# Performance work log

Measured on AMD Instinct MI355X. Metric: run time of the kernel, lower is better.

Reference implementation:

```python
import jax, jax.numpy as jnp
import numpy as np

B, C, T, V = 64, 64, 128, 25   # batch, in_channels, frames, joints
R = 8                          # rel_channels = in_channels // rel_reduction
TS = 9                         # time_step (temporal taps of dynamic adjacency)
OUT = 64                       # out_channels (conv3)


def setup_inputs() -> dict:
    key = jax.random.key(0)
    ks = jax.random.split(key, 10)
    p = lambda k, shape: jax.random.normal(k, shape, jnp.float32) * 0.05
    return {
        'x':  jax.random.normal(ks[0], (B, C, T, V), jnp.float32),
        'A':  jax.random.normal(ks[1], (V, V), jnp.float32) * 0.1,
        'W1': p(ks[2], (R, C)),       'b1': p(ks[3], (R,)),
        'W2': p(ks[4], (R, C)),       'b2': p(ks[5], (R,)),
        'W4': p(ks[6], (C * TS, R)),  'b4': p(ks[7], (C * TS,)),
        'W3': p(ks[8], (OUT, C)),     'b3': p(ks[9], (OUT,)),
    }


def reference(x, A, W1, b1, W2, b2, W4, b4, W3, b3):
    alpha = 1.0
    # conv1/conv2: 1x1 Conv2d then mean over time (dim -2). 1x1 conv is linear,
    # so mean(conv(x)) == einsum/T + bias.  -> (B, R, V)
    x1 = jnp.einsum('rc,bctv->brv', W1, x) / T + b1[None, :, None]
    x2 = jnp.einsum('rc,bctv->brv', W2, x) / T + b2[None, :, None]
    # tanh relation: (B, R, V, 1) - (B, R, 1, V) -> (B, R, V, V)
    rel = jnp.tanh(x1[:, :, :, None] - x2[:, :, None, :])
    # conv4 (1x1): rel_channels -> C*TS dynamic adjacency, + static A
    Adyn = jnp.einsum('or,brij->boij', W4, rel) + b4[None, :, None, None]
    Adyn = Adyn * alpha + A[None, None]                      # (B, C*TS, V, V)
    # reshape(B, C, TS, V, V).permute(0,1,3,4,2): per-(b,c) temporal graph kernel
    Wk = Adyn.reshape(B, C, TS, V, V).transpose(0, 1, 3, 4, 2)  # (B, C, V, V, TS)
    # x -> (B, C, V, T), causal left-pad by TS-1 (matches F.pad(x, (TS-1, 0)))
    xp = jnp.pad(x.transpose(0, 1, 3, 2), ((0, 0), (0, 0), (0, 0), (TS - 1, 0)))
    # Grouped conv1d loop over V vertices, fused into TS tap-wise einsums:
    # z[b,c,t,i] = sum_{v,k} xp[b,c,v,t+k] * Wk[b,c,v,i,k]   (stride=1)
    z = jnp.zeros((B, C, T, V), x.dtype)
    for k in range(TS):  # small fixed tap loop
        z = z + jnp.einsum('bcvt,bcvi->bcti', xp[..., k:k + T], Wk[..., k])
    # conv3: 1x1 Conv2d C -> OUT
    out = jnp.einsum('oc,bctv->botv', W3, z) + b3[None, :, None, None]
    return out
```

## Files before the change

### kernel.cpp

```cpp
#include <hip/hip_runtime.h>
#include <hip/hip_bf16.h>

#define BB 64
#define CC 64
#define TT_ 128
#define VV 25
#define RR 8
#define TS_ 9
#define OO 64

typedef __hip_bfloat16 bf16;
typedef __attribute__((ext_vector_type(8))) short short8;
typedef __attribute__((ext_vector_type(4))) float f32x4;

__device__ __forceinline__ unsigned short f2b(float f) {
    bf16 h = __float2bfloat16(f);
    return __builtin_bit_cast(unsigned short, h);
}

__global__ __launch_bounds__(256) void k_mean(const float* __restrict__ x,
                                              float* __restrict__ xm) {
    __shared__ float sm[256];
    int bc = blockIdx.x;
    int tid = threadIdx.x;
    const float* p = x + (size_t)bc * TT_ * VV;
    float s = 0.f;
    if (tid < 250) {
        for (int off = tid; off < TT_ * VV; off += 250) s += p[off];
    }
    sm[tid] = s;
    __syncthreads();
    if (tid < VV) {
        float tot = 0.f;
        #pragma unroll
        for (int g = 0; g < 10; g++) tot += sm[g * VV + tid];
        xm[bc * VV + tid] = tot * (1.0f / TT_);
    }
}

__global__ __launch_bounds__(256) void k_rel(const float* __restrict__ xm,
                                             const float* __restrict__ W1,
                                             const float* __restrict__ b1,
                                             const float* __restrict__ W2,
                                             const float* __restrict__ b2,
                                             float* __restrict__ rel,
                                             const float* __restrict__ W3,
                                             const float* __restrict__ b3,
                                             float* __restrict__ w3t,
                                             float* __restrict__ b3f) {
    int tid = threadIdx.x;
    if (blockIdx.x >= BB) {
        int idx = (blockIdx.x - BB) * 256 + tid;
        if (idx < OO * CC) {
            int o = idx / CC, c = idx % CC;
            w3t[c * OO + o] = W3[idx];
        }
        if (idx < OO) b3f[idx] = b3[idx];
        return;
    }
    __shared__ float x1s[RR][VV];
    __shared__ float x2s[RR][VV];
    int b = blockIdx.x;
    for (int idx = tid; idx < RR * VV; idx += 256) {
        int r = idx / VV, v = idx % VV;
        float s1 = b1[r], s2 = b2[r];
        for (int c = 0; c < CC; c++) {
            float xv = xm[(b * CC + c) * VV + v];
            s1 += W1[r * CC + c] * xv;
            s2 += W2[r * CC + c] * xv;
        }
        x1s[r][v] = s1;
        x2s[r][v] = s2;
    }
    __syncthreads();
    float* relb = rel + (size_t)b * VV * VV * RR;
    for (int idx = tid; idx < VV * VV * RR; idx += 256) {
        int r = idx % RR;
        int i = (idx / RR) % VV;
        int v = idx / (RR * VV);
        relb[idx] = tanhf(x1s[r][v] - x2s[r][i]);
    }
}

__global__ __launch_bounds__(256) void k_z(const float* __restrict__ x,
                                           const float* __restrict__ Ag,
                                           const float* __restrict__ W4,
                                           const float* __restrict__ b4,
                                           const float* __restrict__ rel,
                                           bf16* __restrict__ zws) {
    __shared__ __align__(16) unsigned short xpadB[136 * 40];
    __shared__ __align__(16) unsigned short AdbS[TS_ * 32 * 40];
    __shared__ float w4l[TS_][RR];
    __shared__ float b4l[TS_];

    int tid = threadIdx.x;
    int bc = blockIdx.x;
    int b = bc / CC, c = bc % CC;

    if (tid < TS_ * RR)
        w4l[tid / RR][tid % RR] = W4[(c * TS_ + tid / RR) * RR + tid % RR];
    if (tid < TS_) b4l[tid] = b4[c * TS_ + tid];

    if (tid < 128) ((unsigned int*)xpadB)[(tid >> 4) * 20 + (tid & 15)] = 0u;
    for (int id = tid; id < 128 * 7; id += 256) {
        int r = 8 + id / 7, v = 25 + id % 7;
        xpadB[r * 40 + v] = 0;
    }
    for (int id = tid; id < TS_ * 25 * 7; id += 256) {
        int s = id / 175, rem = id % 175;
        int i = rem / 7, v = 25 + rem % 7;
        AdbS[(s * 32 + i) * 40 + v] = 0;
    }
    for (int id = tid; id < TS_ * 7 * 16; id += 256) {
        int s = id / 112, rem = id % 112;
        int i = 25 + rem / 16, u = rem % 16;
        ((unsigned int*)AdbS)[(s * 32 + i) * 20 + u] = 0u;
    }
    const float4* xg4 = (const float4*)(x + (size_t)bc * TT_ * VV);
    for (int i4 = tid; i4 < TT_ * VV / 4; i4 += 256) {
        float4 f = xg4[i4];
        int idx = i4 * 4;
        float fe[4] = {f.x, f.y, f.z, f.w};
        #pragma unroll
        for (int e = 0; e < 4; e++) {
            int t = (idx + e) / VV, v = (idx + e) % VV;
            xpadB[(t + 8) * 40 + v] = f2b(fe[e]);
        }
    }
    __syncthreads();

    const float* relb = rel + (size_t)b * VV * VV * RR;
    for (int task = tid; task < VV * VV; task += 256) {
        int v = task / VV, i = task % VV;
        const float4* r4 = (const float4*)(relb + (size_t)task * RR);
        float4 ra = r4[0], rb_ = r4[1];
        float av = Ag[task];
        #pragma unroll
        for (int s = 0; s < TS_; s++) {
            float a2 = b4l[s] + av;
            a2 += w4l[s][0] * ra.x + w4l[s][1] * ra.y + w4l[s][2] * ra.z + w4l[s][3] * ra.w;
            a2 += w4l[s][4] * rb_.x + w4l[s][5] * rb_.y + w4l[s][6] * rb_.z + w4l[s][7] * rb_.w;
            AdbS[(s * 32 + i) * 40 + v] = f2b(a2);
        }
    }
    __syncthreads();

    int lane = tid & 63, wv = tid >> 6;
    int ml = lane & 15, qd = lane >> 4;
    f32x4 acc00 = {0.f, 0.f, 0.f, 0.f};
    f32x4 acc01 = acc00, acc10 = acc00, acc11 = acc00;
    int rowA0 = (wv * 2) * 16 + ml;
    #pragma unroll
    for (int s = 0; s < TS_; s++) {
        short8 a0 = *(const short8*)&xpadB[(rowA0 + s) * 40 + qd * 8];
        short8 a1 = *(const short8*)&xpadB[(rowA0 + 16 + s) * 40 + qd * 8];
        short8 b0 = *(const short8*)&AdbS[(s * 32 + ml) * 40 + qd * 8];
        short8 b1 = *(const short8*)&AdbS[(s * 32 + 16 + ml) * 40 + qd * 8];
        acc00 = __builtin_amdgcn_mfma_f32_16x16x32_bf16(a0, b0, acc00, 0, 0, 0);
        acc01 = __builtin_amdgcn_mfma_f32_16x16x32_bf16(a0, b1, acc01, 0, 0, 0);
        acc10 = __builtin_amdgcn_mfma_f32_16x16x32_bf16(a1, b0, acc10, 0, 0, 0);
        acc11 = __builtin_amdgcn_mfma_f32_16x16x32_bf16(a1, b1, acc11, 0, 0, 0);
    }

    bf16* zb = zws + (size_t)bc * TT_ * VV;
    int t0 = (wv * 2) * 16 + qd * 4;
    int i0 = ml, i1 = 16 + ml;
    #pragma unroll
    for (int r = 0; r < 4; r++) {
        zb[(t0 + r) * VV + i0]      = __float2bfloat16(acc00[r]);
        zb[(t0 + 16 + r) * VV + i0] = __float2bfloat16(acc10[r]);
    }
    if (i1 < VV) {
        #pragma unroll
        for (int r = 0; r < 4; r++) {
            zb[(t0 + r) * VV + i1]      = __float2bfloat16(acc01[r]);
            zb[(t0 + 16 + r) * VV + i1] = __float2bfloat16(acc11[r]);
        }
    }
}

__global__ __launch_bounds__(256) void k_conv3(const bf16* __restrict__ zws,
                                               const float* __restrict__ w3t,
                                               const float* __restrict__ b3f,
                                               float* __restrict__ out) {
    __shared__ float zl[CC][128];
    __shared__ float w3l[CC * OO];
    int tid = threadIdx.x;
    int b = blockIdx.x / 25, tile = blockIdx.x % 25;
    int tj0 = tile * 128;

    for (int idx = tid; idx < CC * OO; idx += 256) w3l[idx] = w3t[idx];
    for (int idx = tid; idx < CC * 128; idx += 256) {
        int c = idx >> 7, j = idx & 127;
        zl[c][j] = __bfloat162float(zws[(size_t)(b * CC + c) * (TT_ * VV) + tj0 + j]);
    }
    __syncthreads();

    int og = tid >> 5, tg = tid & 31;
    int o0 = og * 8, j0 = tg * 4;
    float accv[8][4];
    #pragma unroll
    for (int a = 0; a < 8; a++)
        #pragma unroll
        for (int q = 0; q < 4; q++) accv[a][q] = 0.f;

    for (int c = 0; c < CC; c++) {
        float4 zv = *(const float4*)&zl[c][j0];
        float4 wa = *(const float4*)&w3l[c * OO + o0];
        float4 wb = *(const float4*)&w3l[c * OO + o0 + 4];
        float zq[4] = {zv.x, zv.y, zv.z, zv.w};
        float wo[8] = {wa.x, wa.y, wa.z, wa.w, wb.x, wb.y, wb.z, wb.w};
        #pragma unroll
        for (int a = 0; a < 8; a++)
            #pragma unroll
            for (int q = 0; q < 4; q++) accv[a][q] += wo[a] * zq[q];
    }

    #pragma unroll
    for (int a = 0; a < 8; a++) {
        int o = o0 + a;
        float bo = b3f[o];
        float4 res;
        res.x = accv[a][0] + bo;
        res.y = accv[a][1] + bo;
        res.z = accv[a][2] + bo;
        res.w = accv[a][3] + bo;
        *(float4*)(out + ((size_t)(b * OO + o)) * (TT_ * VV) + tj0 + j0) = res;
    }
}

extern "C" void kernel_launch(void* const* d_in, const int* in_sizes, int n_in,
                              void* d_out, int out_size, void* d_ws, size_t ws_size,
                              hipStream_t stream) {
    const float* x  = (const float*)d_in[0];
    const float* A  = (const float*)d_in[1];
    const float* W1 = (const float*)d_in[2];
    const float* b1 = (const float*)d_in[3];
    const float* W2 = (const float*)d_in[4];
    const float* b2 = (const float*)d_in[5];
    const float* W4 = (const float*)d_in[6];
    const float* b4 = (const float*)d_in[7];
    const float* W3 = (const float*)d_in[8];
    const float* b3 = (const float*)d_in[9];
    float* out = (float*)d_out;

    char* ws = (char*)d_ws;
    float* xm   = (float*)(ws);
    float* rel  = (float*)(ws + 409600);
    float* w3t  = (float*)(ws + 1689600);
    float* b3f  = (float*)(ws + 1705984);
    bf16*  zws  = (bf16*)(ws + 1706240);

    k_mean <<<BB * CC, 256, 0, stream>>>(x, xm);
    k_rel  <<<BB + 16, 256, 0, stream>>>(xm, W1, b1, W2, b2, rel, W3, b3, w3t, b3f);
    k_z    <<<BB * CC, 256, 0, stream>>>(x, A, W4, b4, rel, zws);
    k_conv3<<<BB * 25, 256, 0, stream>>>(zws, w3t, b3f, out);
}
```

Baseline: 194.8 us.

## Use bf16 MFMA for conv3 and drop weight-prep work from rel and z kernels

The 1x1 output conv (k_conv3) moves from a scalar fp32 FMA loop to bf16 16x16x32 MFMA tiles. It converts W3 to bf16 in shared memory inside the kernel and stages z as raw bf16 pairs. This removes the separate W3 transpose and bias copy that k_rel used to do in extra blocks. k_z now reads W4 and b4 straight from global instead of staging them in shared memory. It also drops one barrier and the zero-fill of the unused padding rows of the adjacency tile, whose results are never stored. The cost is lower precision from rounding W3 to bf16, plus narrower output stores: 16 contiguous floats per lane group instead of float4 per thread.

```diff
diff --git a/kernel.cpp b/kernel.cpp
--- a/kernel.cpp
+++ b/kernel.cpp
@@ -43,24 +43,10 @@
                                              const float* __restrict__ b1,
                                              const float* __restrict__ W2,
                                              const float* __restrict__ b2,
-                                             float* __restrict__ rel,
-                                             const float* __restrict__ W3,
-                                             const float* __restrict__ b3,
-                                             float* __restrict__ w3t,
-                                             float* __restrict__ b3f) {
-    int tid = threadIdx.x;
-    if (blockIdx.x >= BB) {
-        int idx = (blockIdx.x - BB) * 256 + tid;
-        if (idx < OO * CC) {
-            int o = idx / CC, c = idx % CC;
-            w3t[c * OO + o] = W3[idx];
-        }
-        if (idx < OO) b3f[idx] = b3[idx];
-        return;
-    }
+                                             float* __restrict__ rel) {
     __shared__ float x1s[RR][VV];
     __shared__ float x2s[RR][VV];
-    int b = blockIdx.x;
+    int b = blockIdx.x, tid = threadIdx.x;
     for (int idx = tid; idx < RR * VV; idx += 256) {
         int r = idx / VV, v = idx % VV;
         float s1 = b1[r], s2 = b2[r];
@@ -90,16 +76,10 @@
                                            bf16* __restrict__ zws) {
     __shared__ __align__(16) unsigned short xpadB[136 * 40];
     __shared__ __align__(16) unsigned short AdbS[TS_ * 32 * 40];
-    __shared__ float w4l[TS_][RR];
-    __shared__ float b4l[TS_];
 
     int tid = threadIdx.x;
     int bc = blockIdx.x;
     int b = bc / CC, c = bc % CC;
-
-    if (tid < TS_ * RR)
-        w4l[tid / RR][tid % RR] = W4[(c * TS_ + tid / RR) * RR + tid % RR];
-    if (tid < TS_) b4l[tid] = b4[c * TS_ + tid];
 
     if (tid < 128) ((unsigned int*)xpadB)[(tid >> 4) * 20 + (tid & 15)] = 0u;
     for (int id = tid; id < 128 * 7; id += 256) {
@@ -110,11 +90,6 @@
         int s = id / 175, rem = id % 175;
         int i = rem / 7, v = 25 + rem % 7;
         AdbS[(s * 32 + i) * 40 + v] = 0;
-    }
-    for (int id = tid; id < TS_ * 7 * 16; id += 256) {
-        int s = id / 112, rem = id % 112;
-        int i = 25 + rem / 16, u = rem % 16;
-        ((unsigned int*)AdbS)[(s * 32 + i) * 20 + u] = 0u;
     }
     const float4* xg4 = (const float4*)(x + (size_t)bc * TT_ * VV);
     for (int i4 = tid; i4 < TT_ * VV / 4; i4 += 256) {
@@ -127,9 +102,10 @@
             xpadB[(t + 8) * 40 + v] = f2b(fe[e]);
         }
     }
-    __syncthreads();
 
     const float* relb = rel + (size_t)b * VV * VV * RR;
+    const float* W4c = W4 + c * TS_ * RR;
+    const float* b4c = b4 + c * TS_;
     for (int task = tid; task < VV * VV; task += 256) {
         int v = task / VV, i = task % VV;
         const float4* r4 = (const float4*)(relb + (size_t)task * RR);
@@ -137,9 +113,11 @@
         float av = Ag[task];
         #pragma unroll
         for (int s = 0; s < TS_; s++) {
-            float a2 = b4l[s] + av;
-            a2 += w4l[s][0] * ra.x + w4l[s][1] * ra.y + w4l[s][2] * ra.z + w4l[s][3] * ra.w;
-            a2 += w4l[s][4] * rb_.x + w4l[s][5] * rb_.y + w4l[s][6] * rb_.z + w4l[s][7] * rb_.w;
+            float a2 = b4c[s] + av;
+            a2 += W4c[s*8+0] * ra.x  + W4c[s*8+1] * ra.y
+                + W4c[s*8+2] * ra.z  + W4c[s*8+3] * ra.w;
+            a2 += W4c[s*8+4] * rb_.x + W4c[s*8+5] * rb_.y
+                + W4c[s*8+6] * rb_.z + W4c[s*8+7] * rb_.w;
             AdbS[(s * 32 + i) * 40 + v] = f2b(a2);
         }
     }
@@ -180,53 +158,68 @@
 }
 
 __global__ __launch_bounds__(256) void k_conv3(const bf16* __restrict__ zws,
-                                               const float* __restrict__ w3t,
-                                               const float* __restrict__ b3f,
+                                               const float* __restrict__ W3,
+                                               const float* __restrict__ b3,
                                                float* __restrict__ out) {
-    __shared__ float zl[CC][128];
-    __shared__ float w3l[CC * OO];
+    __shared__ __align__(16) unsigned short w3b[OO * 72];
+    __shared__ __align__(16) unsigned short zl[CC * 130];
+    __shared__ float b3l[OO];
     int tid = threadIdx.x;
     int b = blockIdx.x / 25, tile = blockIdx.x % 25;
     int tj0 = tile * 128;
 
-    for (int idx = tid; idx < CC * OO; idx += 256) w3l[idx] = w3t[idx];
-    for (int idx = tid; idx < CC * 128; idx += 256) {
-        int c = idx >> 7, j = idx & 127;
-        zl[c][j] = __bfloat162float(zws[(size_t)(b * CC + c) * (TT_ * VV) + tj0 + j]);
-    }
-    __syncthreads();
-
-    int og = tid >> 5, tg = tid & 31;
-    int o0 = og * 8, j0 = tg * 4;
-    float accv[8][4];
-    #pragma unroll
-    for (int a = 0; a < 8; a++)
-        #pragma unroll
-        for (int q = 0; q < 4; q++) accv[a][q] = 0.f;
-
-    for (int c = 0; c < CC; c++) {
-        float4 zv = *(const float4*)&zl[c][j0];
-        float4 wa = *(const float4*)&w3l[c * OO + o0];
-        float4 wb = *(const float4*)&w3l[c * OO + o0 + 4];
-        float zq[4] = {zv.x, zv.y, zv.z, zv.w};
-        float wo[8] = {wa.x, wa.y, wa.z, wa.w, wb.x, wb.y, wb.z, wb.w};
-        #pragma unroll
-        for (int a = 0; a < 8; a++)
+    if (tid < OO) b3l[tid] = b3[tid];
+    for (int idx = tid; idx < OO * CC; idx += 256) {
+        int o = idx >> 6, c = idx & 63;
+        w3b[o * 72 + c] = f2b(W3[idx]);
+    }
+    const unsigned int* zg = (const unsigned int*)(zws + (size_t)b * CC * (TT_ * VV));
+    for (int idu = tid; idu < CC * 64; idu += 256) {
+        int c = idu >> 6, ju = idu & 63;
+        ((unsigned int*)zl)[c * 65 + ju] = zg[c * 1600 + (tj0 >> 1) + ju];
+    }
+    __syncthreads();
+
+    int lane = tid & 63, wv = tid >> 6;
+    int ml = lane & 15, qd = lane >> 4;
+    f32x4 acc[4][2];
+    #pragma unroll
+    for (int m = 0; m < 4; m++)
+        #pragma unroll
+        for (int nl = 0; nl < 2; nl++) acc[m][nl] = (f32x4){0.f, 0.f, 0.f, 0.f};
+
+    #pragma unroll
+    for (int k0 = 0; k0 < 2; k0++) {
+        short8 a[4];
+        #pragma unroll
+        for (int m = 0; m < 4; m++)
+            a[m] = *(const short8*)&w3b[(m * 16 + ml) * 72 + k0 * 32 + qd * 8];
+        #pragma unroll
+        for (int nl = 0; nl < 2; nl++) {
+            int col = (2 * wv + nl) * 16 + ml;
+            int cb = k0 * 32 + qd * 8;
+            short8 bf;
             #pragma unroll
-            for (int q = 0; q < 4; q++) accv[a][q] += wo[a] * zq[q];
-    }
-
-    #pragma unroll
-    for (int a = 0; a < 8; a++) {
-        int o = o0 + a;
-        float bo = b3f[o];
-        float4 res;
-        res.x = accv[a][0] + bo;
-        res.y = accv[a][1] + bo;
-        res.z = accv[a][2] + bo;
-        res.w = accv[a][3] + bo;
-        *(float4*)(out + ((size_t)(b * OO + o)) * (TT_ * VV) + tj0 + j0) = res;
-    }
+            for (int j = 0; j < 8; j++)
+                bf[j] = (short)zl[(cb + j) * 130 + col];
+            #pragma unroll
+            for (int m = 0; m < 4; m++)
+                acc[m][nl] = __builtin_amdgcn_mfma_f32_16x16x32_bf16(a[m], bf, acc[m][nl], 0, 0, 0);
+        }
+    }
+
+    float* ob = out + (size_t)b * OO * (TT_ * VV) + tj0;
+    #pragma unroll
+    for (int m = 0; m < 4; m++)
+        #pragma unroll
+        for (int nl = 0; nl < 2; nl++) {
+            int col = (2 * wv + nl) * 16 + ml;
+            #pragma unroll
+            for (int r = 0; r < 4; r++) {
+                int o = m * 16 + qd * 4 + r;
+                ob[(size_t)o * (TT_ * VV) + col] = acc[m][nl][r] + b3l[o];
+            }
+        }
 }
 
 extern "C" void kernel_launch(void* const* d_in, const int* in_sizes, int n_in,
@@ -247,12 +240,10 @@
     char* ws = (char*)d_ws;
     float* xm   = (float*)(ws);
     float* rel  = (float*)(ws + 409600);
-    float* w3t  = (float*)(ws + 1689600);
-    float* b3f  = (float*)(ws + 1705984);
-    bf16*  zws  = (bf16*)(ws + 1706240);
+    bf16*  zws  = (bf16*)(ws + 1689600);
 
     k_mean <<<BB * CC, 256, 0, stream>>>(x, xm);
-    k_rel  <<<BB + 16, 256, 0, stream>>>(xm, W1, b1, W2, b2, rel, W3, b3, w3t, b3f);
+    k_rel  <<<BB,      256, 0, stream>>>(xm, W1, b1, W2, b2, rel);
     k_z    <<<BB * CC, 256, 0, stream>>>(x, A, W4, b4, rel, zws);
-    k_conv3<<<BB * 25, 256, 0, stream>>>(zws, w3t, b3f, out);
-}
+    k_conv3<<<BB * 25, 256, 0, stream>>>(zws, W3, b3, out);
+}
```

After: 174.0 us. 1.12x faster.
